# Optimization experiments

Measured on AMD Instinct MI355X. Metric: run time of the kernel, lower is better.

Reference implementation:

```python
import jax, jax.numpy as jnp
import numpy as np

N_SAMPLES = 524288
N_FEATURES = 64
N_GATES = 64
N_OUTPUTS = 8
BASE = N_FEATURES + 2                # X cols + constant-0 col + constant-1 col
MAX_CONN = BASE + N_GATES            # 130
TEMPERATURE = 1.0                    # forward() default
NEG = -1e9                           # mask value for not-yet-available slots


def setup_inputs() -> dict:
    key = jax.random.key(0)
    k1, k2, k3 = jax.random.split(key, 3)
    X = jax.random.uniform(k1, (N_SAMPLES, N_FEATURES), dtype=jnp.float32)
    gate_weights = jax.random.normal(k2, (N_GATES, MAX_CONN), dtype=jnp.float32) * 0.1
    output_weights = jax.random.normal(k3, (N_GATES, N_OUTPUTS), dtype=jnp.float32) * 0.1
    output_scale = jnp.ones((N_OUTPUTS,), dtype=jnp.float32)
    return {"X": X, "gate_weights": gate_weights,
            "output_weights": output_weights, "output_scale": output_scale}


def reference(X, gate_weights, output_weights, output_scale):
    n = X.shape[0]
    # available = [X | zeros | ones | gate slots]; gate slots filled sequentially
    buf = jnp.concatenate([
        X,
        jnp.zeros((n, 1), X.dtype),
        jnp.ones((n, 1), X.dtype),
        jnp.zeros((n, N_GATES), X.dtype),
    ], axis=1)                                            # [N, MAX_CONN]

    # Connection selection is data-independent: softmax over the first
    # (BASE + gate_idx) slots of each gate's weight row, then top-2.
    col_ids = jnp.arange(MAX_CONN)
    avail_mask = col_ids[None, :] < (BASE + jnp.arange(N_GATES))[:, None]
    logits = jnp.where(avail_mask, gate_weights / TEMPERATURE, NEG)
    probs = jax.nn.softmax(logits, axis=1)                # [n_gates, MAX_CONN]
    _, top2 = jax.lax.top_k(probs, 2)                     # [n_gates, 2]

    # Sequential NAND chain over a small fixed number of gates (structural loop).
    gate_outs = []
    for i in range(N_GATES):
        a = buf[:, top2[i, 0]]                            # [N]
        b = buf[:, top2[i, 1]]
        g = 1.0 - a * b                                   # continuous NAND
        gate_outs.append(g)
        buf = buf.at[:, BASE + i].set(g)

    gate_matrix = jnp.stack(gate_outs, axis=1)            # [N, n_gates]
    outputs = (gate_matrix @ output_weights) * output_scale
    return outputs
```

## Files before the change

### kernel.cpp

```cpp
#include <hip/hip_runtime.h>
#include <hip/hip_fp16.h>

#define N_SAMPLES 524288
#define N_FEATURES 64
#define N_GATES 64
#define N_OUTPUTS 8
#define BASE_COLS 66
#define MAX_CONN 130

#define NWAVES 8
#define MAXW 256
#define ROWS 131
#define GWS_STR 131
#define PAD_SLOT (64 | (64 << 8) | (130 << 16))

typedef float v2f __attribute__((ext_vector_type(2)));

__device__ __forceinline__ void top2_ins(float x, int j, float& v1, int& i1, float& v2, int& i2) {
    bool gt1 = (x > v1) || (x == v1 && j < i1);
    bool gt2 = (x > v2) || (x == v2 && j < i2);
    if (gt1) { v2 = v1; i2 = i1; v1 = x; i1 = j; }
    else if (gt2) { v2 = x; i2 = j; }
}

__global__ __launch_bounds__(256) void plan_kernel(
    const float* __restrict__ gw,
    int* __restrict__ stream)
{
    __shared__ float gws[N_GATES * GWS_STR];
    __shared__ float pv1[4][N_GATES], pv2[4][N_GATES];
    __shared__ int   pi1[4][N_GATES], pi2[4][N_GATES];
    __shared__ int   streamL[NWAVES * MAXW];

    const int tid = threadIdx.x;

    const float4* gw4 = (const float4*)gw;
    for (int k = tid; k < (N_GATES * MAX_CONN) / 4; k += 256) {
        float4 v = gw4[k];
        int base = 4 * k;
        #pragma unroll
        for (int e = 0; e < 4; ++e) {
            int idx = base + e;
            int gi  = idx / MAX_CONN;
            int jj  = idx - gi * MAX_CONN;
            gws[gi * GWS_STR + jj] = (&v.x)[e];
        }
    }
    __syncthreads();

    {
        const int g = tid & 63, s = tid >> 6;
        const int avail = BASE_COLS + g;
        int j0 = s * 33;
        int j1 = j0 + 33; if (j1 > avail) j1 = avail;
        float v1 = -1e30f, v2 = -1e30f;
        int   i1 = 0x7fffffff, i2 = 0x7fffffff;
        const float* w = gws + g * GWS_STR;
        for (int j = j0; j < j1; ++j)
            top2_ins(w[j], j, v1, i1, v2, i2);
        pv1[s][g] = v1; pi1[s][g] = i1;
        pv2[s][g] = v2; pi2[s][g] = i2;
    }
    __syncthreads();

    if (tid >= 64) return;
    const int l = tid;

    float v1 = -1e30f, v2 = -1e30f;
    int   i1 = 0x7fffffff, i2 = 0x7fffffff;
    #pragma unroll
    for (int s = 0; s < 4; ++s) {
        top2_ins(pv1[s][l], pi1[s][l], v1, i1, v2, i2);
        top2_ins(pv2[s][l], pi2[s][l], v1, i1, v2, i2);
    }

    const bool ga = (i1 >= BASE_COLS), gb = (i2 >= BASE_COLS);
    const int  pa = ga ? (i1 - BASE_COLS) : 0;
    const int  pb = gb ? (i2 - BASE_COLS) : 0;
    int lvl = 0;
    bool changed = true;
    while (__any(changed)) {
        int la = __shfl(lvl, pa);
        int lb = __shfl(lvl, pb);
        int nl = lvl;
        if (ga && la + 1 > nl) nl = la + 1;
        if (gb && lb + 1 > nl) nl = lb + 1;
        changed = (nl != lvl);
        lvl = nl;
    }

    for (int q = l; q < NWAVES * MAXW; q += 64) streamL[q] = -2;

    int p_base = 0, assigned = 0;
    int myW = 0, myP = 0;
    for (int L = 0; L < 64 && assigned < 64; ++L) {
        unsigned long long mask = __ballot(lvl == L);
        int c = __popcll(mask);
        if (!c) continue;
        int m  = (c + NWAVES - 1) >> 3;
        int mp = (m + 1) & ~1;
        if (lvl == L) {
            int r = __popcll(mask & ((1ull << l) - 1ull));
            myW = r & 7; myP = p_base + (r >> 3);
        }
        if (l <= mp) {
            int val = (l == mp) ? -1 : PAD_SLOT;
            #pragma unroll
            for (int wv = 0; wv < NWAVES; ++wv)
                streamL[wv * MAXW + p_base + l] = val;
        }
        p_base += mp + 1;
        assigned += c;
    }

    streamL[myW * MAXW + myP] = i1 | (i2 << 8) | ((BASE_COLS + l) << 16) | (l << 24);

    for (int q = l; q < NWAVES * MAXW; q += 64) stream[q] = streamL[q];
}

__global__ __launch_bounds__(512, 6) void circuit_kernel(
    const float* __restrict__ X,
    const int*   __restrict__ stream,
    const float* __restrict__ ow,
    const float* __restrict__ scale,
    float*       __restrict__ out)
{
    __shared__ __align__(16) __half2 buf[ROWS * 64];

    const int tid = threadIdx.x;
    const int w = tid >> 6, t = tid & 63;
    const long long s0 = (long long)blockIdx.x * 128;

    const int* st = stream + w * MAXW;
    const int sv0 = st[t], sv1 = st[64 + t], sv2 = st[128 + t], sv3 = st[192 + t];

    const float4* Xv = (const float4*)(X + s0 * N_FEATURES);
    #pragma unroll
    for (int k = 0; k < 2; ++k) {
        int q  = k * 512 + tid;
        int c4 = q & 15;
        int j  = q >> 4;
        float4 va = Xv[(2 * j)     * 16 + c4];
        float4 vb = Xv[(2 * j + 1) * 16 + c4];
        int c = 4 * c4;
        buf[(c + 0) * 64 + (j ^ ((c + 0) & 31))] = __halves2half2(__float2half(va.x), __float2half(vb.x));
        buf[(c + 1) * 64 + (j ^ ((c + 1) & 31))] = __halves2half2(__float2half(va.y), __float2half(vb.y));
        buf[(c + 2) * 64 + (j ^ ((c + 2) & 31))] = __halves2half2(__float2half(va.z), __float2half(vb.z));
        buf[(c + 3) * 64 + (j ^ ((c + 3) & 31))] = __halves2half2(__float2half(va.w), __float2half(vb.w));
    }
    if (tid < 64)        buf[64 * 64 + tid]              = __half2half2(__float2half(0.0f));
    else if (tid < 128)  buf[65 * 64 + ((tid - 64) ^ 1)] = __half2half2(__float2half(1.0f));
    __syncthreads();

    const __half2 one2 = __half2half2(__float2half(1.0f));
    v2f acc[N_OUTPUTS];
    #pragma unroll
    for (int o = 0; o < N_OUTPUTS; ++o) { acc[o].x = 0.0f; acc[o].y = 0.0f; }

    #define FETCH(P) ((P) < 128 \
        ? ((P) < 64  ? __builtin_amdgcn_readlane(sv0, (P))       : __builtin_amdgcn_readlane(sv1, (P) - 64)) \
        : ((P) < 192 ? __builtin_amdgcn_readlane(sv2, (P) - 128) : __builtin_amdgcn_readlane(sv3, (P) - 192)))

    int p = 0;
    while (true) {
        int sa = FETCH(p);
        if (sa < 0) {
            ++p;
            if (sa == -1) { __syncthreads(); continue; }
            break;
        }
        int sb = FETCH(p + 1);
        p += 2;

        const int ra0 =  sa        & 255, rb0 = (sa >> 8) & 255;
        const int wr0 = (sa >> 16) & 255, g0  = (sa >> 24) & 63;
        const int ra1 =  sb        & 255, rb1 = (sb >> 8) & 255;
        const int wr1 = (sb >> 16) & 255, g1  = (sb >> 24) & 63;

        __half2 a0 = buf[ra0 * 64 + (t ^ (ra0 & 31))];
        __half2 b0 = buf[rb0 * 64 + (t ^ (rb0 & 31))];
        __half2 a1 = buf[ra1 * 64 + (t ^ (ra1 & 31))];
        __half2 b1 = buf[rb1 * 64 + (t ^ (rb1 & 31))];

        __half2 v0 = __hfma2(__hneg2(a0), b0, one2);
        __half2 v1 = __hfma2(__hneg2(a1), b1, one2);
        buf[wr0 * 64 + (t ^ (wr0 & 31))] = v0;
        buf[wr1 * 64 + (t ^ (wr1 & 31))] = v1;

        if (wr0 != 130) {
            v2f g2; g2.x = __low2float(v0); g2.y = __high2float(v0);
            #pragma unroll
            for (int o = 0; o < N_OUTPUTS; ++o) {
                float wt = ow[g0 * N_OUTPUTS + o];
                v2f wv; wv.x = wt; wv.y = wt;
                acc[o] = __builtin_elementwise_fma(g2, wv, acc[o]);
            }
        }
        if (wr1 != 130) {
            v2f g2; g2.x = __low2float(v1); g2.y = __high2float(v1);
            #pragma unroll
            for (int o = 0; o < N_OUTPUTS; ++o) {
                float wt = ow[g1 * N_OUTPUTS + o];
                v2f wv; wv.x = wt; wv.y = wt;
                acc[o] = __builtin_elementwise_fma(g2, wv, acc[o]);
            }
        }
    }
    #undef FETCH

    __syncthreads();
    float2* red = (float2*)buf;
    #pragma unroll
    for (int o = 0; o < N_OUTPUTS; ++o) {
        float2 v; v.x = acc[o].x; v.y = acc[o].y;
        red[w * 512 + o * 64 + t] = v;
    }
    __syncthreads();
    #pragma unroll
    for (int k = 0; k < 4; ++k) {
        int f = k * 512 + tid;
        float2 a = red[f], b = red[f + 2048];
        a.x += b.x; a.y += b.y; red[f] = a;
    }
    __syncthreads();
    #pragma unroll
    for (int k = 0; k < 2; ++k) {
        int f = k * 512 + tid;
        float2 a = red[f], b = red[f + 1024];
        a.x += b.x; a.y += b.y; red[f] = a;
    }
    __syncthreads();
    {
        int f = tid;
        float2 a = red[f], b = red[f + 512];
        a.x += b.x; a.y += b.y; red[f] = a;
    }
    __syncthreads();

    if (w == 0) {
        float sc[N_OUTPUTS];
        #pragma unroll
        for (int o = 0; o < N_OUTPUTS; ++o) sc[o] = scale[o];

        float2 s[N_OUTPUTS];
        #pragma unroll
        for (int o = 0; o < N_OUTPUTS; ++o) {
            float2 r = red[o * 64 + t];
            s[o].x = r.x * sc[o]; s[o].y = r.y * sc[o];
        }
        float4* outv = (float4*)(out + (s0 + 2 * t) * N_OUTPUTS);
        outv[0] = make_float4(s[0].x, s[1].x, s[2].x, s[3].x);
        outv[1] = make_float4(s[4].x, s[5].x, s[6].x, s[7].x);
        outv[2] = make_float4(s[0].y, s[1].y, s[2].y, s[3].y);
        outv[3] = make_float4(s[4].y, s[5].y, s[6].y, s[7].y);
    }
}

extern "C" void kernel_launch(void* const* d_in, const int* in_sizes, int n_in,
                              void* d_out, int out_size, void* d_ws, size_t ws_size,
                              hipStream_t stream_)
{
    const float* X     = (const float*)d_in[0];
    const float* gw    = (const float*)d_in[1];
    const float* ow    = (const float*)d_in[2];
    const float* scale = (const float*)d_in[3];
    float* out = (float*)d_out;

    int* stream_ws = (int*)d_ws;

    plan_kernel<<<1, 256, 0, stream_>>>(gw, stream_ws);

    const int blocks = N_SAMPLES / 128;
    circuit_kernel<<<blocks, 512, 0, stream_>>>(X, stream_ws, ow, scale, out);
}
```

Baseline: 230.5 us.

## Process four samples per lane with paired half2 and synthesize constant columns

Each lane now handles four samples, stored as two half2 values per slot, so each block covers 256 samples and the per-gate stream decode, readlane and control overhead is spread over twice as many samples. The constant zero and one columns are no longer stored in shared memory; reads of those columns are replaced with register constants. Padding slots are marked by a sentinel gate index so their writes are skipped, and the XOR swizzle is changed to suit 8-byte entries. The cost is twice the shared memory and accumulator registers per block, and the occupancy hint drops from 6 to 4 blocks.

New measurement: 241.2 us. 4.6% more time.

```diff
diff --git a/kernel.cpp b/kernel.cpp
--- a/kernel.cpp
+++ b/kernel.cpp
@@ -10,11 +10,12 @@
 
 #define NWAVES 8
 #define MAXW 256
-#define ROWS 131
 #define GWS_STR 131
-#define PAD_SLOT (64 | (64 << 8) | (130 << 16))
+#define PAD_SLOT (64 | (64 << 8) | (255 << 16))
 
 typedef float v2f __attribute__((ext_vector_type(2)));
+
+struct __align__(8) H22 { __half2 lo, hi; };
 
 __device__ __forceinline__ void top2_ins(float x, int j, float& v1, int& i1, float& v2, int& i2) {
     bool gt1 = (x > v1) || (x == v1 && j < i1);
@@ -113,23 +114,23 @@
         assigned += c;
     }
 
-    streamL[myW * MAXW + myP] = i1 | (i2 << 8) | ((BASE_COLS + l) << 16) | (l << 24);
+    streamL[myW * MAXW + myP] = i1 | (i2 << 8) | (l << 16);
 
     for (int q = l; q < NWAVES * MAXW; q += 64) stream[q] = streamL[q];
 }
 
-__global__ __launch_bounds__(512, 6) void circuit_kernel(
+__global__ __launch_bounds__(512, 4) void circuit_kernel(
     const float* __restrict__ X,
     const int*   __restrict__ stream,
     const float* __restrict__ ow,
     const float* __restrict__ scale,
     float*       __restrict__ out)
 {
-    __shared__ __align__(16) __half2 buf[ROWS * 64];
+    __shared__ H22 buf[128 * 64];
 
     const int tid = threadIdx.x;
     const int w = tid >> 6, t = tid & 63;
-    const long long s0 = (long long)blockIdx.x * 128;
+    const long long s0 = (long long)blockIdx.x * 256;
 
     const int* st = stream + w * MAXW;
     const int sv0 = st[t], sv1 = st[64 + t], sv2 = st[128 + t], sv3 = st[192 + t];
@@ -140,26 +141,41 @@
         int q  = k * 512 + tid;
         int c4 = q & 15;
         int j  = q >> 4;
-        float4 va = Xv[(2 * j)     * 16 + c4];
-        float4 vb = Xv[(2 * j + 1) * 16 + c4];
-        int c = 4 * c4;
-        buf[(c + 0) * 64 + (j ^ ((c + 0) & 31))] = __halves2half2(__float2half(va.x), __float2half(vb.x));
-        buf[(c + 1) * 64 + (j ^ ((c + 1) & 31))] = __halves2half2(__float2half(va.y), __float2half(vb.y));
-        buf[(c + 2) * 64 + (j ^ ((c + 2) & 31))] = __halves2half2(__float2half(va.z), __float2half(vb.z));
-        buf[(c + 3) * 64 + (j ^ ((c + 3) & 31))] = __halves2half2(__float2half(va.w), __float2half(vb.w));
-    }
-    if (tid < 64)        buf[64 * 64 + tid]              = __half2half2(__float2half(0.0f));
-    else if (tid < 128)  buf[65 * 64 + ((tid - 64) ^ 1)] = __half2half2(__float2half(1.0f));
-    __syncthreads();
-
-    const __half2 one2 = __half2half2(__float2half(1.0f));
-    v2f acc[N_OUTPUTS];
-    #pragma unroll
-    for (int o = 0; o < N_OUTPUTS; ++o) { acc[o].x = 0.0f; acc[o].y = 0.0f; }
+        float4 va = Xv[(4 * j)     * 16 + c4];
+        float4 vb = Xv[(4 * j + 1) * 16 + c4];
+        float4 vc = Xv[(4 * j + 2) * 16 + c4];
+        float4 vd = Xv[(4 * j + 3) * 16 + c4];
+        #pragma unroll
+        for (int i = 0; i < 4; ++i) {
+            int c = 4 * c4 + i;
+            H22 v;
+            v.lo = __halves2half2(__float2half((&va.x)[i]), __float2half((&vb.x)[i]));
+            v.hi = __halves2half2(__float2half((&vc.x)[i]), __float2half((&vd.x)[i]));
+            buf[c * 64 + (j ^ c4)] = v;
+        }
+    }
+    __syncthreads();
+
+    const __half2 one2  = __half2half2(__float2half(1.0f));
+    const __half2 zero2 = __half2half2(__float2half(0.0f));
+
+    v2f accA[N_OUTPUTS], accB[N_OUTPUTS];
+    #pragma unroll
+    for (int o = 0; o < N_OUTPUTS; ++o) {
+        accA[o].x = 0.0f; accA[o].y = 0.0f;
+        accB[o].x = 0.0f; accB[o].y = 0.0f;
+    }
 
     #define FETCH(P) ((P) < 128 \
         ? ((P) < 64  ? __builtin_amdgcn_readlane(sv0, (P))       : __builtin_amdgcn_readlane(sv1, (P) - 64)) \
         : ((P) < 192 ? __builtin_amdgcn_readlane(sv2, (P) - 128) : __builtin_amdgcn_readlane(sv3, (P) - 192)))
+
+    #define RD(e, dst) do {                                                    \
+        int _row = ((e) >= BASE_COLS) ? ((e) - 2) : (((e) < 64) ? (e) : 0);    \
+        dst = buf[_row * 64 + (t ^ ((_row >> 2) & 15))];                       \
+        if ((e) == 64)      { dst.lo = zero2; dst.hi = zero2; }                \
+        else if ((e) == 65) { dst.lo = one2;  dst.hi = one2;  }                \
+    } while (0)
 
     int p = 0;
     while (true) {
@@ -172,68 +188,76 @@
         int sb = FETCH(p + 1);
         p += 2;
 
-        const int ra0 =  sa        & 255, rb0 = (sa >> 8) & 255;
-        const int wr0 = (sa >> 16) & 255, g0  = (sa >> 24) & 63;
-        const int ra1 =  sb        & 255, rb1 = (sb >> 8) & 255;
-        const int wr1 = (sb >> 16) & 255, g1  = (sb >> 24) & 63;
-
-        __half2 a0 = buf[ra0 * 64 + (t ^ (ra0 & 31))];
-        __half2 b0 = buf[rb0 * 64 + (t ^ (rb0 & 31))];
-        __half2 a1 = buf[ra1 * 64 + (t ^ (ra1 & 31))];
-        __half2 b1 = buf[rb1 * 64 + (t ^ (rb1 & 31))];
-
-        __half2 v0 = __hfma2(__hneg2(a0), b0, one2);
-        __half2 v1 = __hfma2(__hneg2(a1), b1, one2);
-        buf[wr0 * 64 + (t ^ (wr0 & 31))] = v0;
-        buf[wr1 * 64 + (t ^ (wr1 & 31))] = v1;
-
-        if (wr0 != 130) {
-            v2f g2; g2.x = __low2float(v0); g2.y = __high2float(v0);
+        const int ea0 =  sa        & 255, eb0 = (sa >> 8) & 255, g0 = (sa >> 16) & 255;
+        const int ea1 =  sb        & 255, eb1 = (sb >> 8) & 255, g1 = (sb >> 16) & 255;
+
+        H22 a0, b0, a1, b1;
+        RD(ea0, a0); RD(eb0, b0); RD(ea1, a1); RD(eb1, b1);
+
+        H22 v0, v1;
+        v0.lo = __hfma2(__hneg2(a0.lo), b0.lo, one2);
+        v0.hi = __hfma2(__hneg2(a0.hi), b0.hi, one2);
+        v1.lo = __hfma2(__hneg2(a1.lo), b1.lo, one2);
+        v1.hi = __hfma2(__hneg2(a1.hi), b1.hi, one2);
+
+        if (g0 != 255) {
+            int row = 64 + g0;
+            buf[row * 64 + (t ^ ((row >> 2) & 15))] = v0;
+            v2f glo, ghi;
+            glo.x = __low2float(v0.lo); glo.y = __high2float(v0.lo);
+            ghi.x = __low2float(v0.hi); ghi.y = __high2float(v0.hi);
             #pragma unroll
             for (int o = 0; o < N_OUTPUTS; ++o) {
                 float wt = ow[g0 * N_OUTPUTS + o];
                 v2f wv; wv.x = wt; wv.y = wt;
-                acc[o] = __builtin_elementwise_fma(g2, wv, acc[o]);
+                accA[o] = __builtin_elementwise_fma(glo, wv, accA[o]);
+                accB[o] = __builtin_elementwise_fma(ghi, wv, accB[o]);
             }
         }
-        if (wr1 != 130) {
-            v2f g2; g2.x = __low2float(v1); g2.y = __high2float(v1);
+        if (g1 != 255) {
+            int row = 64 + g1;
+            buf[row * 64 + (t ^ ((row >> 2) & 15))] = v1;
+            v2f glo, ghi;
+            glo.x = __low2float(v1.lo); glo.y = __high2float(v1.lo);
+            ghi.x = __low2float(v1.hi); ghi.y = __high2float(v1.hi);
             #pragma unroll
             for (int o = 0; o < N_OUTPUTS; ++o) {
                 float wt = ow[g1 * N_OUTPUTS + o];
                 v2f wv; wv.x = wt; wv.y = wt;
-                acc[o] = __builtin_elementwise_fma(g2, wv, acc[o]);
+                accA[o] = __builtin_elementwise_fma(glo, wv, accA[o]);
+                accB[o] = __builtin_elementwise_fma(ghi, wv, accB[o]);
             }
         }
     }
     #undef FETCH
-
-    __syncthreads();
-    float2* red = (float2*)buf;
+    #undef RD
+
+    __syncthreads();
+    float4* red = (float4*)buf;
     #pragma unroll
     for (int o = 0; o < N_OUTPUTS; ++o) {
-        float2 v; v.x = acc[o].x; v.y = acc[o].y;
+        float4 v; v.x = accA[o].x; v.y = accA[o].y; v.z = accB[o].x; v.w = accB[o].y;
         red[w * 512 + o * 64 + t] = v;
     }
     __syncthreads();
     #pragma unroll
     for (int k = 0; k < 4; ++k) {
         int f = k * 512 + tid;
-        float2 a = red[f], b = red[f + 2048];
-        a.x += b.x; a.y += b.y; red[f] = a;
+        float4 a = red[f], b = red[f + 2048];
+        a.x += b.x; a.y += b.y; a.z += b.z; a.w += b.w; red[f] = a;
     }
     __syncthreads();
     #pragma unroll
     for (int k = 0; k < 2; ++k) {
         int f = k * 512 + tid;
-        float2 a = red[f], b = red[f + 1024];
-        a.x += b.x; a.y += b.y; red[f] = a;
+        float4 a = red[f], b = red[f + 1024];
+        a.x += b.x; a.y += b.y; a.z += b.z; a.w += b.w; red[f] = a;
     }
     __syncthreads();
     {
         int f = tid;
-        float2 a = red[f], b = red[f + 512];
-        a.x += b.x; a.y += b.y; red[f] = a;
+        float4 a = red[f], b = red[f + 512];
+        a.x += b.x; a.y += b.y; a.z += b.z; a.w += b.w; red[f] = a;
     }
     __syncthreads();
 
@@ -242,17 +266,18 @@
         #pragma unroll
         for (int o = 0; o < N_OUTPUTS; ++o) sc[o] = scale[o];
 
-        float2 s[N_OUTPUTS];
+        float4 F[N_OUTPUTS];
         #pragma unroll
         for (int o = 0; o < N_OUTPUTS; ++o) {
-            float2 r = red[o * 64 + t];
-            s[o].x = r.x * sc[o]; s[o].y = r.y * sc[o];
-        }
-        float4* outv = (float4*)(out + (s0 + 2 * t) * N_OUTPUTS);
-        outv[0] = make_float4(s[0].x, s[1].x, s[2].x, s[3].x);
-        outv[1] = make_float4(s[4].x, s[5].x, s[6].x, s[7].x);
-        outv[2] = make_float4(s[0].y, s[1].y, s[2].y, s[3].y);
-        outv[3] = make_float4(s[4].y, s[5].y, s[6].y, s[7].y);
+            F[o] = red[o * 64 + t];
+            F[o].x *= sc[o]; F[o].y *= sc[o]; F[o].z *= sc[o]; F[o].w *= sc[o];
+        }
+        float4* outv = (float4*)(out + (s0 + 4 * t) * N_OUTPUTS);
+        #pragma unroll
+        for (int i = 0; i < 4; ++i) {
+            outv[i * 2 + 0] = make_float4((&F[0].x)[i], (&F[1].x)[i], (&F[2].x)[i], (&F[3].x)[i]);
+            outv[i * 2 + 1] = make_float4((&F[4].x)[i], (&F[5].x)[i], (&F[6].x)[i], (&F[7].x)[i]);
+        }
     }
 }
 
@@ -270,6 +295,6 @@
 
     plan_kernel<<<1, 256, 0, stream_>>>(gw, stream_ws);
 
-    const int blocks = N_SAMPLES / 128;
+    const int blocks = N_SAMPLES / 256;
     circuit_kernel<<<blocks, 512, 0, stream_>>>(X, stream_ws, ow, scale, out);
 }
```
